# Performance work log

Hardware: AMD Instinct MI355X
Metric: run time of the kernel (lower is better)

The kernel has to match this reference:

```python
import jax, jax.numpy as jnp
import numpy as np

N_HEADS = 8
N_HIDDEN = 32  # out_features // n_heads
NEG_SLOPE = 0.21
MASK_VAL = -1000000.0  # precision == '32'


def setup_inputs() -> dict:
    key = jax.random.key(0)
    k1, k2, k3, k4, k5 = jax.random.split(key, 5)
    B, N, Fin = 4, 512, 256
    HF = N_HEADS * N_HIDDEN
    h = jax.random.normal(k1, (B, N, Fin), dtype=jnp.float32)
    adj_mat = jax.random.randint(k2, (1, N, N, 1), 0, 2, dtype=jnp.int32)
    W_l = jax.random.normal(k3, (Fin, HF), dtype=jnp.float32) * 0.05
    W_r = jax.random.normal(k4, (Fin, HF), dtype=jnp.float32) * 0.05
    attn_w = jax.random.normal(k5, (N_HIDDEN,), dtype=jnp.float32) * 0.05
    return {"h": h, "adj_mat": adj_mat, "W_l": W_l, "W_r": W_r, "attn_w": attn_w}


def reference(h, adj_mat, W_l, W_r, attn_w):
    B, N, _ = h.shape
    H, F = N_HEADS, N_HIDDEN
    g_l = (h @ W_l).reshape(B, N, H, F)
    g_r = (h @ W_r).reshape(B, N, H, F)
    # torch repeat/repeat_interleave semantics: g_sum[b,i,j] = g_l[b,j] + g_r[b,i]
    g_sum = g_l[:, None, :, :, :] + g_r[:, :, None, :, :]  # (B, i, j, H, F)
    act = jnp.where(g_sum >= 0, g_sum, NEG_SLOPE * g_sum)
    e = jnp.einsum('bijhf,f->bijh', act, attn_w)  # (B, N, N, H)
    e = jnp.where(adj_mat == 0, MASK_VAL, e)
    a = jax.nn.softmax(e, axis=2)
    # dropout is identity in eval mode
    attn_res = jnp.einsum('bijh,bjhf->bihf', a, g_r)
    return attn_res.reshape(B, N, H * F)  # is_concat=True
```

## Files before the change

kernel.cpp:

```cpp
#include <hip/hip_runtime.h>
#include <math.h>

#define BB 4
#define NN 512
#define FIN 256
#define NH 8
#define FD 32
#define HF 256
#define CA 0.8728305f
#define CB 0.5698645f
#define IT 32
#define ESTR 268
#define GTS 260
#define GLX(j) ((j) ^ (((j) >> 5) & 7))
#define ALX(j) ((j) + ((j) >> 5))

typedef _Float16 h2_t __attribute__((ext_vector_type(2)));
union H2U { unsigned u; h2_t h; };
typedef __fp16 v8h __attribute__((ext_vector_type(8)));
typedef float v4f __attribute__((ext_vector_type(4)));
union U8 { uint4 u4; v8h h; };

__device__ __forceinline__ h2_t pkrtz(float a, float b) {
  auto r = __builtin_amdgcn_cvt_pkrtz(a, b);
  union { decltype(r) f; h2_t h; } u;
  u.f = r;
  return u.h;
}
__device__ __forceinline__ unsigned pkrtz_u(float a, float b) {
  H2U u; u.h = pkrtz(a, b);
  return u.u;
}

__device__ __forceinline__ float acc2(unsigned g, h2_t q, h2_t u, float acc) {
  H2U v; v.u = g;
  h2_t s = v.h + q;
  H2U a; a.h = s; a.u &= 0x7fff7fffu;
  return __builtin_amdgcn_fdot2(a.h, u, acc, false);
}

__device__ __forceinline__ float score16(uint4 g0, uint4 g1, uint4 g2, uint4 g3,
                                         const h2_t* qh, const h2_t* uh,
                                         float init) {
  float e0 = init, e1 = 0.f;
  e0 = acc2(g0.x, qh[0], uh[0], e0);
  e1 = acc2(g0.y, qh[1], uh[1], e1);
  e0 = acc2(g0.z, qh[2], uh[2], e0);
  e1 = acc2(g0.w, qh[3], uh[3], e1);
  e0 = acc2(g1.x, qh[4], uh[4], e0);
  e1 = acc2(g1.y, qh[5], uh[5], e1);
  e0 = acc2(g1.z, qh[6], uh[6], e0);
  e1 = acc2(g1.w, qh[7], uh[7], e1);
  e0 = acc2(g2.x, qh[8], uh[8], e0);
  e1 = acc2(g2.y, qh[9], uh[9], e1);
  e0 = acc2(g2.z, qh[10], uh[10], e0);
  e1 = acc2(g2.w, qh[11], uh[11], e1);
  e0 = acc2(g3.x, qh[12], uh[12], e0);
  e1 = acc2(g3.y, qh[13], uh[13], e1);
  e0 = acc2(g3.z, qh[14], uh[14], e0);
  e1 = acc2(g3.w, qh[15], uh[15], e1);
  return e0 + e1;
}

__global__ __launch_bounds__(256) void gemm_dual(
    const float* __restrict__ h, const float* __restrict__ Wl,
    const float* __restrict__ Wr, _Float16* __restrict__ glh,
    _Float16* __restrict__ grh) {
  const int t = threadIdx.x;
  const int row0 = blockIdx.x * 8;
  const float* __restrict__ W = blockIdx.y ? Wr : Wl;

  float acc[8] = {0.f, 0.f, 0.f, 0.f, 0.f, 0.f, 0.f, 0.f};
  const float* Wp = W + t;
  const float* hp = h + (size_t)row0 * FIN;

#pragma unroll 2
  for (int k4 = 0; k4 < FIN / 4; ++k4) {
    float4 hv[8];
#pragma unroll
    for (int r = 0; r < 8; ++r)
      hv[r] = *(const float4*)(hp + r * FIN + 4 * k4);
#pragma unroll
    for (int kk = 0; kk < 4; ++kk) {
      const float w = Wp[(size_t)(4 * k4 + kk) * HF];
#pragma unroll
      for (int r = 0; r < 8; ++r) {
        const float hval = (kk == 0) ? hv[r].x
                         : (kk == 1) ? hv[r].y
                         : (kk == 2) ? hv[r].z : hv[r].w;
        acc[r] = fmaf(hval, w, acc[r]);
      }
    }
  }

  _Float16* gp = (blockIdx.y ? grh : glh) + (size_t)row0 * HF + t;
#pragma unroll
  for (int r = 0; r < 8; ++r) gp[(size_t)r * HF] = (_Float16)acc[r];
}

__global__ __launch_bounds__(512, 4) void gat_attn(
    const _Float16* __restrict__ glh, const _Float16* __restrict__ grh,
    const int* __restrict__ adj, const float* __restrict__ aw,
    float* __restrict__ out) {
  __shared__ __align__(16) unsigned ubuf[32 * GTS];
  __shared__ __align__(16) unsigned e_s[IT][ESTR];
  __shared__ float Al_s[544];
  __shared__ float s_part[32][33];
  __shared__ float inv_l[IT];

  const int t = threadIdx.x;
  const int hh = blockIdx.x;
  const int i0 = blockIdx.y * IT;
  const int b = blockIdx.z;
  const int r0 = t & 15;
  const int jg = t >> 4;

  uint4* gl4 = (uint4*)ubuf;

  const _Float16* glp = glh + (size_t)b * NN * HF + hh * FD;

  h2_t wv[16], uh[16], qh[16], qh2[16];
  float a_r0 = 0.f, a_r1 = 0.f;
  {
#pragma unroll
    for (int f4 = 0; f4 < 8; ++f4) {
      const float4 w4 = *(const float4*)(aw + 4 * f4);
      wv[2 * f4] = pkrtz(CA * w4.x, CA * w4.y);
      wv[2 * f4 + 1] = pkrtz(CA * w4.z, CA * w4.w);
      uh[2 * f4] = pkrtz(CB * w4.x, CB * w4.y);
      uh[2 * f4 + 1] = pkrtz(CB * w4.z, CB * w4.w);
    }
    const uint4* qa =
        (const uint4*)(grh + (size_t)(b * NN + i0 + r0) * HF + hh * FD);
    const uint4* qb =
        (const uint4*)(grh + (size_t)(b * NN + i0 + r0 + 16) * HF + hh * FD);
    const uint4 q0 = qa[0], q1 = qa[1], q2 = qa[2], q3 = qa[3];
    const uint4 p0 = qb[0], p1 = qb[1], p2 = qb[2], p3 = qb[3];
    H2U z;
    z.u = q0.x; qh[0] = z.h;  z.u = q0.y; qh[1] = z.h;
    z.u = q0.z; qh[2] = z.h;  z.u = q0.w; qh[3] = z.h;
    z.u = q1.x; qh[4] = z.h;  z.u = q1.y; qh[5] = z.h;
    z.u = q1.z; qh[6] = z.h;  z.u = q1.w; qh[7] = z.h;
    z.u = q2.x; qh[8] = z.h;  z.u = q2.y; qh[9] = z.h;
    z.u = q2.z; qh[10] = z.h; z.u = q2.w; qh[11] = z.h;
    z.u = q3.x; qh[12] = z.h; z.u = q3.y; qh[13] = z.h;
    z.u = q3.z; qh[14] = z.h; z.u = q3.w; qh[15] = z.h;
    z.u = p0.x; qh2[0] = z.h;  z.u = p0.y; qh2[1] = z.h;
    z.u = p0.z; qh2[2] = z.h;  z.u = p0.w; qh2[3] = z.h;
    z.u = p1.x; qh2[4] = z.h;  z.u = p1.y; qh2[5] = z.h;
    z.u = p1.z; qh2[6] = z.h;  z.u = p1.w; qh2[7] = z.h;
    z.u = p2.x; qh2[8] = z.h;  z.u = p2.y; qh2[9] = z.h;
    z.u = p2.z; qh2[10] = z.h; z.u = p2.w; qh2[11] = z.h;
    z.u = p3.x; qh2[12] = z.h; z.u = p3.y; qh2[13] = z.h;
    z.u = p3.z; qh2[14] = z.h; z.u = p3.w; qh2[15] = z.h;
#pragma unroll
    for (int f2 = 0; f2 < 16; ++f2) {
      a_r0 = __builtin_amdgcn_fdot2(qh[f2], wv[f2], a_r0, false);
      a_r1 = __builtin_amdgcn_fdot2(qh2[f2], wv[f2], a_r1, false);
    }
  }

  {
    const int j = t;
    const uint4* gp = (const uint4*)(glp + (size_t)j * HF);
    const uint4 g0 = gp[0], g1 = gp[1], g2 = gp[2], g3 = gp[3];
    const int jx = GLX(j);
    gl4[0 * NN + jx] = g0;
    gl4[1 * NN + jx] = g1;
    gl4[2 * NN + jx] = g2;
    gl4[3 * NN + jx] = g3;
    float s0 = 0.f, s1 = 0.f;
    H2U v;
#define ALD(gu, i)                                                  \
  v.u = gu.x; s0 = __builtin_amdgcn_fdot2(v.h, wv[i+0], s0, false); \
  v.u = gu.y; s1 = __builtin_amdgcn_fdot2(v.h, wv[i+1], s1, false); \
  v.u = gu.z; s0 = __builtin_amdgcn_fdot2(v.h, wv[i+2], s0, false); \
  v.u = gu.w; s1 = __builtin_amdgcn_fdot2(v.h, wv[i+3], s1, false);
    ALD(g0, 0) ALD(g1, 4) ALD(g2, 8) ALD(g3, 12)
#undef ALD
    Al_s[ALX(j)] = s0 + s1;
  }
  __syncthreads();

  {
    unsigned* erow0 = &e_s[r0][jg * 8];
    unsigned* erow1 = &e_s[r0 + 16][jg * 8];
    const int* adjp0 = adj + (size_t)(i0 + r0) * NN + jg * 16;
    const int* adjp1 = adj + (size_t)(i0 + r0 + 16) * NN + jg * 16;
    float srow0 = 0.f, srow1 = 0.f;
#pragma unroll 2
    for (int g4 = 0; g4 < 4; ++g4) {
      const int4 m0 = ((const int4*)adjp0)[g4];
      const int4 m1 = ((const int4*)adjp1)[g4];
      float p0[4], p1[4];
#pragma unroll
      for (int k = 0; k < 4; ++k) {
        const int j = jg * 16 + 4 * g4 + k;
        const int jx = GLX(j);
        const uint4 g0 = gl4[0 * NN + jx], g1 = gl4[1 * NN + jx];
        const uint4 g2 = gl4[2 * NN + jx], g3 = gl4[3 * NN + jx];
        const float al = Al_s[ALX(j)];
        const float e0 = score16(g0, g1, g2, g3, qh, uh, al + a_r0);
        const float e1 = score16(g0, g1, g2, g3, qh2, uh, al + a_r1);
        const int mk = (k == 0) ? m0.x : (k == 1) ? m0.y : (k == 2) ? m0.z : m0.w;
        const int nk = (k == 0) ? m1.x : (k == 1) ? m1.y : (k == 2) ? m1.z : m1.w;
        p0[k] = mk ? __builtin_amdgcn_exp2f(e0) : 0.f;
        p1[k] = nk ? __builtin_amdgcn_exp2f(e1) : 0.f;
      }
      srow0 += (p0[0] + p0[1]) + (p0[2] + p0[3]);
      srow1 += (p1[0] + p1[1]) + (p1[2] + p1[3]);
      uint2 w0, w1;
      w0.x = pkrtz_u(p0[0], p0[1]);
      w0.y = pkrtz_u(p0[2], p0[3]);
      w1.x = pkrtz_u(p1[0], p1[1]);
      w1.y = pkrtz_u(p1[2], p1[3]);
      *(uint2*)&erow0[2 * g4] = w0;
      *(uint2*)&erow1[2 * g4] = w1;
    }
    s_part[jg][r0] = srow0;
    s_part[jg][r0 + 16] = srow1;
  }
  __syncthreads();

  {
    const int fq = t & 7;
    const int jp0 = t >> 3;
    const unsigned* gbase =
        (const unsigned*)(grh + (size_t)b * NN * HF + hh * FD) + 2 * fq;
#pragma unroll
    for (int s2 = 0; s2 < 4; ++s2) {
      const int jp = jp0 + 64 * s2;
      const uint2 A = *(const uint2*)(gbase + (size_t)(2 * jp) * 128);
      const uint2 Bv = *(const uint2*)(gbase + (size_t)(2 * jp + 1) * 128);
      ubuf[(4 * fq + 0) * GTS + jp] = __builtin_amdgcn_perm(Bv.x, A.x, 0x05040100u);
      ubuf[(4 * fq + 1) * GTS + jp] = __builtin_amdgcn_perm(Bv.x, A.x, 0x07060302u);
      ubuf[(4 * fq + 2) * GTS + jp] = __builtin_amdgcn_perm(Bv.y, A.y, 0x05040100u);
      ubuf[(4 * fq + 3) * GTS + jp] = __builtin_amdgcn_perm(Bv.y, A.y, 0x07060302u);
    }
    if (t < IT) {
      float s = 0.f;
#pragma unroll
      for (int c = 0; c < 32; ++c) s += s_part[c][t];
      inv_l[t] = 1.f / s;
    }
  }
  __syncthreads();

  if (t < 256) {
    const int lane = t & 63;
    const int wv3 = t >> 6;
    const int Mt = wv3 & 1, Nt = wv3 >> 1;
    const int l16 = lane & 15, q = lane >> 4;
    const unsigned* arow = &e_s[Mt * 16 + l16][0];
    const unsigned* brow = &ubuf[(Nt * 16 + l16) * GTS];
    v4f acc = {0.f, 0.f, 0.f, 0.f};
#pragma unroll
    for (int s = 0; s < 16; ++s) {
      U8 a; a.u4 = *(const uint4*)(arow + 16 * s + 4 * q);
      U8 bf; bf.u4 = *(const uint4*)(brow + 16 * s + 4 * q);
      acc = __builtin_amdgcn_mfma_f32_16x16x32_f16(a.h, bf.h, acc, 0, 0, 0);
    }
    float* op = out + (size_t)(b * NN + i0 + Mt * 16 + q * 4) * HF + hh * FD +
                Nt * 16 + l16;
#pragma unroll
    for (int r = 0; r < 4; ++r) {
      op[(size_t)r * HF] = acc[r] * inv_l[Mt * 16 + q * 4 + r];
    }
  }
}

extern "C" void kernel_launch(void* const* d_in, const int* in_sizes, int n_in,
                              void* d_out, int out_size, void* d_ws,
                              size_t ws_size, hipStream_t stream) {
  const float* h = (const float*)d_in[0];
  const int* adj = (const int*)d_in[1];
  const float* Wl = (const float*)d_in[2];
  const float* Wr = (const float*)d_in[3];
  const float* aw = (const float*)d_in[4];
  float* out = (float*)d_out;

  _Float16* glh = (_Float16*)d_ws;
  _Float16* grh = (_Float16*)((char*)d_ws + (size_t)BB * NN * HF * 2);

  dim3 gg(BB * NN / 8, 2, 1);
  gemm_dual<<<gg, 256, 0, stream>>>(h, Wl, Wr, glh, grh);

  dim3 ga(NH, NN / IT, BB);
  gat_attn<<<ga, 512, 0, stream>>>(glh, grh, adj, aw, out);
}
```

Measured before the change: 103.3 us.

## Tile projection GEMM through shared memory with register-prefetched k-slices

Replaces the per-thread 8-row projection GEMM, which streamed W straight from global memory, with a 64x64 output tile per block. Each k-slice of h and W is staged in padded shared memory, and the next slice is prefetched into registers while the current one is computed. Each thread accumulates a 4x4 micro-tile and writes packed fp16 results. The aim is more data reuse and fewer global loads in the GEMM stage. The cost is extra barriers and a smaller grid of 256 blocks, while the attention kernel is left unchanged.

```diff
diff --git a/kernel.cpp b/kernel.cpp
--- a/kernel.cpp
+++ b/kernel.cpp
@@ -14,6 +14,8 @@
 #define GTS 260
 #define GLX(j) ((j) ^ (((j) >> 5) & 7))
 #define ALX(j) ((j) + ((j) >> 5))
+#define KT 64
+#define HS 68
 
 typedef _Float16 h2_t __attribute__((ext_vector_type(2)));
 union H2U { unsigned u; h2_t h; };
@@ -66,36 +68,88 @@
     const float* __restrict__ h, const float* __restrict__ Wl,
     const float* __restrict__ Wr, _Float16* __restrict__ glh,
     _Float16* __restrict__ grh) {
+  __shared__ __align__(16) float hs[KT * HS];
+  __shared__ __align__(16) float ws[KT * HS];
+
   const int t = threadIdx.x;
-  const int row0 = blockIdx.x * 8;
-  const float* __restrict__ W = blockIdx.y ? Wr : Wl;
-
-  float acc[8] = {0.f, 0.f, 0.f, 0.f, 0.f, 0.f, 0.f, 0.f};
-  const float* Wp = W + t;
-  const float* hp = h + (size_t)row0 * FIN;
-
-#pragma unroll 2
-  for (int k4 = 0; k4 < FIN / 4; ++k4) {
-    float4 hv[8];
-#pragma unroll
-    for (int r = 0; r < 8; ++r)
-      hv[r] = *(const float4*)(hp + r * FIN + 4 * k4);
-#pragma unroll
-    for (int kk = 0; kk < 4; ++kk) {
-      const float w = Wp[(size_t)(4 * k4 + kk) * HF];
-#pragma unroll
-      for (int r = 0; r < 8; ++r) {
-        const float hval = (kk == 0) ? hv[r].x
-                         : (kk == 1) ? hv[r].y
-                         : (kk == 2) ? hv[r].z : hv[r].w;
-        acc[r] = fmaf(hval, w, acc[r]);
+  const int rt = blockIdx.x;
+  const int cs = blockIdx.y;
+  const int row0 = rt * 64;
+  const float* __restrict__ W = (cs < 4) ? Wl : Wr;
+  const int c0 = (cs & 3) * 64;
+
+  const int tc = t & 15;
+  const int tr = t >> 4;
+  const int sc = t & 15;
+  const int sk = t >> 4;
+
+  float4 hr[4], wr_[4];
+#pragma unroll
+  for (int i = 0; i < 4; ++i) {
+    hr[i] = *(const float4*)(h + (size_t)(row0 + sk + 16 * i) * FIN + 4 * sc);
+    wr_[i] = *(const float4*)(W + (size_t)(sk + 16 * i) * HF + c0 + 4 * sc);
+  }
+
+  float acc[4][4];
+#pragma unroll
+  for (int i = 0; i < 4; ++i)
+#pragma unroll
+    for (int j = 0; j < 4; ++j) acc[i][j] = 0.f;
+
+  for (int s = 0; s < 4; ++s) {
+    if (s) __syncthreads();
+#pragma unroll
+    for (int i = 0; i < 4; ++i) {
+      *(float4*)&hs[(sk + 16 * i) * HS + 4 * sc] = hr[i];
+      *(float4*)&ws[(sk + 16 * i) * HS + 4 * sc] = wr_[i];
+    }
+    __syncthreads();
+    if (s < 3) {
+      const int k0 = KT * (s + 1);
+#pragma unroll
+      for (int i = 0; i < 4; ++i) {
+        hr[i] = *(const float4*)(h + (size_t)(row0 + sk + 16 * i) * FIN +
+                                 k0 + 4 * sc);
+        wr_[i] = *(const float4*)(W + (size_t)(k0 + sk + 16 * i) * HF +
+                                  c0 + 4 * sc);
       }
     }
-  }
-
-  _Float16* gp = (blockIdx.y ? grh : glh) + (size_t)row0 * HF + t;
-#pragma unroll
-  for (int r = 0; r < 8; ++r) gp[(size_t)r * HF] = (_Float16)acc[r];
+#pragma unroll
+    for (int k4 = 0; k4 < KT / 4; ++k4) {
+      float4 hv[4], wv[4];
+#pragma unroll
+      for (int i = 0; i < 4; ++i)
+        hv[i] = *(const float4*)&hs[(4 * tr + i) * HS + 4 * k4];
+#pragma unroll
+      for (int kk = 0; kk < 4; ++kk)
+        wv[kk] = *(const float4*)&ws[(4 * k4 + kk) * HS + 4 * tc];
+#pragma unroll
+      for (int kk = 0; kk < 4; ++kk) {
+#pragma unroll
+        for (int i = 0; i < 4; ++i) {
+          const float hvk = (kk == 0) ? hv[i].x
+                          : (kk == 1) ? hv[i].y
+                          : (kk == 2) ? hv[i].z : hv[i].w;
+          acc[i][0] = fmaf(hvk, wv[kk].x, acc[i][0]);
+          acc[i][1] = fmaf(hvk, wv[kk].y, acc[i][1]);
+          acc[i][2] = fmaf(hvk, wv[kk].z, acc[i][2]);
+          acc[i][3] = fmaf(hvk, wv[kk].w, acc[i][3]);
+        }
+      }
+    }
+  }
+
+  _Float16* gout = (cs < 4) ? glh : grh;
+#pragma unroll
+  for (int i = 0; i < 4; ++i) {
+    const int row = row0 + 4 * tr + i;
+    h2_t pa, pb;
+    pa[0] = (_Float16)acc[i][0]; pa[1] = (_Float16)acc[i][1];
+    pb[0] = (_Float16)acc[i][2]; pb[1] = (_Float16)acc[i][3];
+    H2U ua, ub; ua.h = pa; ub.h = pb;
+    uint2 o; o.x = ua.u; o.y = ub.u;
+    *(uint2*)(gout + (size_t)row * HF + c0 + 4 * tc) = o;
+  }
 }
 
 __global__ __launch_bounds__(512, 4) void gat_attn(
@@ -282,7 +336,7 @@
   _Float16* glh = (_Float16*)d_ws;
   _Float16* grh = (_Float16*)((char*)d_ws + (size_t)BB * NN * HF * 2);
 
-  dim3 gg(BB * NN / 8, 2, 1);
+  dim3 gg(32, 8, 1);
   gemm_dual<<<gg, 256, 0, stream>>>(h, Wl, Wr, glh, grh);
 
   dim3 ga(NH, NN / IT, BB);
```

After: 102.6 us. No clear change (-0.7%).

## Use split-fp16 MFMA for projection GEMM with LDS-staged weights

Applied to the files above, without the earlier changes.

Replaces the scalar FMA projection GEMM with MFMA 16x16x32 f16 instructions. It keeps near-fp32 accuracy by splitting each operand into high and scaled low fp16 parts and running three MFMAs per tile. Weights are transposed and split into shared memory, and the grid becomes 64-row by 64-column tiles. This cuts the FMA cost of the GEMM stage but adds conversion work, LDS traffic and a smaller grid.

```diff
diff --git a/kernel.cpp b/kernel.cpp
--- a/kernel.cpp
+++ b/kernel.cpp
@@ -14,6 +14,7 @@
 #define GTS 260
 #define GLX(j) ((j) ^ (((j) >> 5) & 7))
 #define ALX(j) ((j) + ((j) >> 5))
+#define WTS 132
 
 typedef _Float16 h2_t __attribute__((ext_vector_type(2)));
 union H2U { unsigned u; h2_t h; };
@@ -30,6 +31,17 @@
 __device__ __forceinline__ unsigned pkrtz_u(float a, float b) {
   H2U u; u.h = pkrtz(a, b);
   return u.u;
+}
+
+__device__ __forceinline__ void split2(float a, float b,
+                                       unsigned& uhi, unsigned& ulo) {
+  const _Float16 ah = (_Float16)a, bh = (_Float16)b;
+  h2_t hi; hi[0] = ah; hi[1] = bh;
+  h2_t lo;
+  lo[0] = (_Float16)((a - (float)ah) * 2048.f);
+  lo[1] = (_Float16)((b - (float)bh) * 2048.f);
+  H2U x, y; x.h = hi; y.h = lo;
+  uhi = x.u; ulo = y.u;
 }
 
 __device__ __forceinline__ float acc2(unsigned g, h2_t q, h2_t u, float acc) {
@@ -66,36 +78,86 @@
     const float* __restrict__ h, const float* __restrict__ Wl,
     const float* __restrict__ Wr, _Float16* __restrict__ glh,
     _Float16* __restrict__ grh) {
+  __shared__ __align__(16) unsigned WTh[64][WTS];
+  __shared__ __align__(16) unsigned WTl[64][WTS];
+
   const int t = threadIdx.x;
-  const int row0 = blockIdx.x * 8;
-  const float* __restrict__ W = blockIdx.y ? Wr : Wl;
-
-  float acc[8] = {0.f, 0.f, 0.f, 0.f, 0.f, 0.f, 0.f, 0.f};
-  const float* Wp = W + t;
-  const float* hp = h + (size_t)row0 * FIN;
-
-#pragma unroll 2
-  for (int k4 = 0; k4 < FIN / 4; ++k4) {
-    float4 hv[8];
-#pragma unroll
-    for (int r = 0; r < 8; ++r)
-      hv[r] = *(const float4*)(hp + r * FIN + 4 * k4);
-#pragma unroll
-    for (int kk = 0; kk < 4; ++kk) {
-      const float w = Wp[(size_t)(4 * k4 + kk) * HF];
-#pragma unroll
-      for (int r = 0; r < 8; ++r) {
-        const float hval = (kk == 0) ? hv[r].x
-                         : (kk == 1) ? hv[r].y
-                         : (kk == 2) ? hv[r].z : hv[r].w;
-        acc[r] = fmaf(hval, w, acc[r]);
+  const int rt = blockIdx.x;
+  const int cs = blockIdx.y;
+  const float* __restrict__ W = (cs < 4) ? Wl : Wr;
+  const int c0 = (cs & 3) * 64;
+
+  const int lane = t & 63;
+  const int wv_ = t >> 6;
+  const int l16 = lane & 15;
+  const int q = lane >> 4;
+  const int row = rt * 64 + wv_ * 16 + l16;
+
+  const float* hp = h + (size_t)row * FIN;
+  float4 ha[16];
+#pragma unroll
+  for (int s = 0; s < 8; ++s) {
+    ha[2 * s]     = *(const float4*)(hp + 32 * s + 8 * q);
+    ha[2 * s + 1] = *(const float4*)(hp + 32 * s + 8 * q + 4);
+  }
+
+  {
+    const int cq = t >> 4;
+    const int kq = t & 15;
+#pragma unroll
+    for (int it = 0; it < 8; ++it) {
+      const int ku = kq + 16 * it;
+      const int k = 2 * ku;
+      const float4 wa = *(const float4*)(W + (size_t)k * HF + c0 + 4 * cq);
+      const float4 wb = *(const float4*)(W + (size_t)(k + 1) * HF + c0 + 4 * cq);
+#pragma unroll
+      for (int n = 0; n < 4; ++n) {
+        const float a = (n == 0) ? wa.x : (n == 1) ? wa.y : (n == 2) ? wa.z : wa.w;
+        const float b = (n == 0) ? wb.x : (n == 1) ? wb.y : (n == 2) ? wb.z : wb.w;
+        unsigned uh_, ul_;
+        split2(a, b, uh_, ul_);
+        WTh[4 * cq + n][ku] = uh_;
+        WTl[4 * cq + n][ku] = ul_;
       }
     }
   }
-
-  _Float16* gp = (blockIdx.y ? grh : glh) + (size_t)row0 * HF + t;
-#pragma unroll
-  for (int r = 0; r < 8; ++r) gp[(size_t)r * HF] = (_Float16)acc[r];
+  __syncthreads();
+
+  v4f accA[4], accB[4];
+#pragma unroll
+  for (int nt = 0; nt < 4; ++nt) {
+    accA[nt] = (v4f){0.f, 0.f, 0.f, 0.f};
+    accB[nt] = (v4f){0.f, 0.f, 0.f, 0.f};
+  }
+#pragma unroll
+  for (int s = 0; s < 8; ++s) {
+    U8 aH, aL;
+    split2(ha[2 * s].x,     ha[2 * s].y,     aH.u4.x, aL.u4.x);
+    split2(ha[2 * s].z,     ha[2 * s].w,     aH.u4.y, aL.u4.y);
+    split2(ha[2 * s + 1].x, ha[2 * s + 1].y, aH.u4.z, aL.u4.z);
+    split2(ha[2 * s + 1].z, ha[2 * s + 1].w, aH.u4.w, aL.u4.w);
+#pragma unroll
+    for (int nt = 0; nt < 4; ++nt) {
+      const int col = nt * 16 + l16;
+      U8 bH, bL;
+      bH.u4 = *(const uint4*)&WTh[col][16 * s + 4 * q];
+      bL.u4 = *(const uint4*)&WTl[col][16 * s + 4 * q];
+      accA[nt] = __builtin_amdgcn_mfma_f32_16x16x32_f16(aH.h, bH.h, accA[nt], 0, 0, 0);
+      accB[nt] = __builtin_amdgcn_mfma_f32_16x16x32_f16(aH.h, bL.h, accB[nt], 0, 0, 0);
+      accB[nt] = __builtin_amdgcn_mfma_f32_16x16x32_f16(aL.h, bH.h, accB[nt], 0, 0, 0);
+    }
+  }
+
+  _Float16* gout = (cs < 4) ? glh : grh;
+  const int orow = rt * 64 + wv_ * 16 + q * 4;
+#pragma unroll
+  for (int nt = 0; nt < 4; ++nt) {
+#pragma unroll
+    for (int r = 0; r < 4; ++r) {
+      const float g = accA[nt][r] + accB[nt][r] * (1.f / 2048.f);
+      gout[(size_t)(orow + r) * HF + c0 + nt * 16 + l16] = (_Float16)g;
+    }
+  }
 }
 
 __global__ __launch_bounds__(512, 4) void gat_attn(
@@ -282,7 +344,7 @@
   _Float16* glh = (_Float16*)d_ws;
   _Float16* grh = (_Float16*)((char*)d_ws + (size_t)BB * NN * HF * 2);
 
-  dim3 gg(BB * NN / 8, 2, 1);
+  dim3 gg(32, 8, 1);
   gemm_dual<<<gg, 256, 0, stream>>>(h, Wl, Wr, glh, grh);
 
   dim3 ga(NH, NN / IT, BB);
```

New measurement: 90.33 us, median of 2. -12.6%, faster.
